# Performance work log

Measured on AMD Instinct MI355X. Metric: run time of the kernel, lower is better.

Reference implementation:

```python
import jax, jax.numpy as jnp
import numpy as np

jax.config.update("jax_enable_x64", True)  # hash uses int64 (prime * coord ~ 7e12)

FEATURE_DIM = 2
GRID_DIM = 3
NUM_LVL = 16
MAX_RES = 2048
MIN_RES = 16
HASH_POWER = 19
MAX_ENTRY = 2 ** HASH_POWER
PRIMES = (3367900313, 2654435761, 805459861)

_b = np.exp((np.log(MAX_RES) - np.log(MIN_RES)) / (NUM_LVL - 1))
RESOLUTIONS = [int(np.floor(MIN_RES * _b ** i)) for i in range(NUM_LVL)]
TABLE_SIZES = [min(r ** GRID_DIM, MAX_ENTRY) for r in RESOLUTIONS]

# Corner offset order matches get_corner(): [c000, c010, c001, c011, c100, c101, c110, c111]
OFFSETS = np.array([[0, 0, 0], [0, 1, 0], [0, 0, 1], [0, 1, 1],
                    [1, 0, 0], [1, 0, 1], [1, 1, 0], [1, 1, 1]], dtype=np.int64)

N = 1 << 20  # number of query points


def setup_inputs() -> dict:
    key = jax.random.key(0)
    kx, kt = jax.random.split(key)
    x = jax.random.uniform(kx, (N, GRID_DIM), dtype=jnp.float32)  # in [0,1]
    # stacked (padded) hashtables; dense levels only use their first res^3 rows
    tables = jax.random.normal(kt, (NUM_LVL, MAX_ENTRY, FEATURE_DIM), dtype=jnp.float32) * 1e-4
    return {"x": x, "tables": tables}


def _level(x, table, res, table_size):
    resf = float(res)
    coord = jnp.clip(x * (resf - 1.0), 0.0, resf - 1.0001)  # [N,3] hash-space coords
    fl = jnp.floor(coord)
    corners = fl.astype(jnp.int64)[:, None, :] + jnp.asarray(OFFSETS)  # [N,8,3]
    if table_size != MAX_ENTRY:
        # dense spatial index: sum_i c_i * res^i
        idx = corners[..., 0] + corners[..., 1] * res + corners[..., 2] * (res * res)
    else:
        # NGP hash: xor of coord*prime, mod table size
        h = (corners[..., 0] * PRIMES[0]) ^ (corners[..., 1] * PRIMES[1]) ^ (corners[..., 2] * PRIMES[2])
        idx = h % MAX_ENTRY
    feat = table[idx]  # [N,8,F] gather
    d = coord - fl  # fractional part, [N,3]
    xx, yy, zz = d[:, 0], d[:, 1], d[:, 2]
    mx, my, mz = 1.0 - xx, 1.0 - yy, 1.0 - zz
    # weight order matches interpolation_weights() stack order
    w = jnp.stack([mx * my * mz, xx * my * mz, mx * yy * mz, xx * yy * mz,
                   mx * my * zz, xx * my * zz, mx * yy * zz, xx * yy * zz], axis=-1)  # [N,8]
    return (feat * w[..., None]).sum(axis=-2)  # [N,F]


def reference(x, tables):
    outs = [_level(x, tables[l], RESOLUTIONS[l], TABLE_SIZES[l]) for l in range(NUM_LVL)]
    return jnp.concatenate(outs, axis=-1)  # [N, NUM_LVL*FEATURE_DIM]
```

## Files before the change

kernel.cpp:

```cpp
#include <hip/hip_runtime.h>
#include <math.h>

#define NLVL 16
#define MAX_ENTRY (1 << 19)
#define NPTS (1 << 20)

typedef float f2_t __attribute__((ext_vector_type(2)));
typedef float f4_t __attribute__((ext_vector_type(4)));

__device__ __forceinline__ void nt_store2(float2 v, float2* p) {
    f2_t t; t.x = v.x; t.y = v.y;
    __builtin_nontemporal_store(t, (f2_t*)p);
}
__device__ __forceinline__ void nt_store4(float4 v, float4* p) {
    f4_t t; t.x = v.x; t.y = v.y; t.z = v.z; t.w = v.w;
    __builtin_nontemporal_store(t, (f4_t*)p);
}
__device__ __forceinline__ void nt_storeu(unsigned v, unsigned* p) {
    __builtin_nontemporal_store(v, p);
}
__device__ __forceinline__ float4 nt_load4(const float4* p) {
    f4_t t = __builtin_nontemporal_load((const f4_t*)p);
    return make_float4(t.x, t.y, t.z, t.w);
}
__device__ __forceinline__ unsigned nt_loadu(const unsigned* p) {
    return __builtin_nontemporal_load(p);
}

__device__ __forceinline__ unsigned pack_bf16(float a, float b) {
    unsigned ua = __float_as_uint(a), ub = __float_as_uint(b);
    ua = (ua + 0x7FFFu + ((ua >> 16) & 1u)) >> 16;
    ub = (ub + 0x7FFFu + ((ub >> 16) & 1u)) >> 16;
    return ua | (ub << 16);
}
__device__ __forceinline__ float bf_lo(unsigned u) { return __uint_as_float(u << 16); }
__device__ __forceinline__ float bf_hi(unsigned u) { return __uint_as_float(u & 0xFFFF0000u); }

__device__ __constant__ int OX[8] = {0, 0, 0, 0, 1, 1, 1, 1};
__device__ __constant__ int OY[8] = {0, 1, 0, 1, 0, 0, 1, 1};
__device__ __constant__ int OZ[8] = {0, 0, 1, 1, 0, 1, 0, 1};

__device__ __forceinline__ void corner_setup(
    float x0, float x1, float x2, float s, float hi,
    int& cx, int& cy, int& cz,
    float (&wx)[2], float (&wy)[2], float (&wz)[2])
{
    float c0 = fminf(fmaxf(x0 * s, 0.0f), hi);
    float c1 = fminf(fmaxf(x1 * s, 0.0f), hi);
    float c2 = fminf(fmaxf(x2 * s, 0.0f), hi);
    float f0 = floorf(c0), f1 = floorf(c1), f2 = floorf(c2);
    cx = (int)f0; cy = (int)f1; cz = (int)f2;
    float xx = c0 - f0, yy = c1 - f1, zz = c2 - f2;
    wx[0] = 1.0f - xx; wx[1] = xx;
    wy[0] = 1.0f - yy; wy[1] = yy;
    wz[0] = 1.0f - zz; wz[1] = zz;
}

__device__ __forceinline__ void acc_pair(
    int j, float4 f, const float (&wx)[2], const float (&wy)[2], const float (&wz)[2],
    float& a0, float& a1)
{
    const float w0 = wx[j & 1] * wy[j >> 1] * wz[0];
    const float w1 = wx[j >> 1] * wy[j & 1] * wz[1];
    a0 += w0 * f.x + w1 * f.z;
    a1 += w0 * f.y + w1 * f.w;
}

struct OptP {
    int   res[NLVL];
    int   res2[NLVL];
    float scale[NLVL];
    float hi[NLVL];
    int   cdim1, cdim2, cdim3;
};


__global__ __launch_bounds__(256) void repack2_kernel(
    const float* __restrict__ x,
    const float* __restrict__ tables,
    float4* __restrict__ blk1,
    float4* __restrict__ blk2,
    float4* __restrict__ blk3,
    float4* __restrict__ xp,
    OptP P)
{
    const long long stride = (long long)gridDim.x * 256;
    const long long tid = (long long)blockIdx.x * 256 + threadIdx.x;

#pragma unroll
    for (int l = 1; l <= 2; ++l) {
        const int res = P.res[l], res2v = P.res2[l];
        const int cdim = res - 1;
        const long long ncell = (long long)cdim * cdim * cdim;
        const float2* tab = (const float2*)(tables + (size_t)l * MAX_ENTRY * 2);
        float4* dst = (l == 1) ? blk1 : blk2;
        for (long long c = tid; c < ncell; c += stride) {
            const int cx = (int)(c % cdim);
            const int cy = (int)((c / cdim) % cdim);
            const int cz = (int)(c / ((long long)cdim * cdim));
            const int base = cx + cy * res + cz * res2v;
#pragma unroll
            for (int j = 0; j < 4; ++j) {
                const int oy = j & 1, oz = j >> 1;
                const float2 e0 = tab[base + oy * res + oz * res2v];
                const float2 e1 = tab[base + 1 + oy * res + oz * res2v];
                nt_store4(make_float4(e0.x, e0.y, e1.x, e1.y), &dst[c * 4 + j]);
            }
        }
    }

    {
        const int res = P.res[3], res2v = P.res2[3];
        const int cdim = P.cdim3;
        const long long nblk = (long long)cdim * cdim * res;
        const float2* tab = (const float2*)(tables + (size_t)3 * MAX_ENTRY * 2);
        for (long long b = tid; b < nblk; b += stride) {
            const int bx = (int)(b % cdim);
            const int by = (int)((b / cdim) % cdim);
            const int z  = (int)(b / ((long long)cdim * cdim));
            const int base = bx + by * res + z * res2v;
#pragma unroll
            for (int oy = 0; oy < 2; ++oy) {
                const float2 e0 = tab[base + oy * res];
                const float2 e1 = tab[base + 1 + oy * res];
                nt_store4(make_float4(e0.x, e0.y, e1.x, e1.y), &blk3[b * 2 + oy]);
            }
        }
    }

    for (long long i = tid; i < NPTS; i += stride) {
        xp[i] = make_float4(x[3 * i + 0], x[3 * i + 1], x[3 * i + 2], 0.0f);
    }
}

__global__ __launch_bounds__(256) void passA_kernel(
    const float4* __restrict__ xp,
    const float* __restrict__ tables,
    const float4* __restrict__ blk1,
    const float4* __restrict__ blk2,
    unsigned* __restrict__ fb,
    OptP P)
{
    __shared__ float2 lds0[4096];
    {
        const float2* tab0 = (const float2*)tables;
        for (int j = threadIdx.x; j < 4096; j += 256) lds0[j] = tab0[j];
    }
    __syncthreads();

    const int i = blockIdx.x * 256 + threadIdx.x;

    const float4 v = nt_load4(&xp[i]);
    const float x0 = v.x, x1 = v.y, x2 = v.z;

    {
        int cx, cy, cz;
        float wx[2], wy[2], wz[2];
        corner_setup(x0, x1, x2, P.scale[0], P.hi[0], cx, cy, cz, wx, wy, wz);
        const int res = P.res[0], res2v = P.res2[0];
        const int base = cx + cy * res + cz * res2v;
        float a0 = 0.0f, a1 = 0.0f;
#pragma unroll
        for (int k = 0; k < 8; ++k) {
            const int idx = base + OX[k] + OY[k] * res + OZ[k] * res2v;
            const float2 f = lds0[idx];
            const float w = wx[k & 1] * wy[(k >> 1) & 1] * wz[k >> 2];
            a0 += w * f.x; a1 += w * f.y;
        }
        nt_storeu(pack_bf16(a0, a1), &fb[i]);
    }

#pragma unroll
    for (int l = 1; l <= 2; ++l) {
        int cx, cy, cz;
        float wx[2], wy[2], wz[2];
        corner_setup(x0, x1, x2, P.scale[l], P.hi[l], cx, cy, cz, wx, wy, wz);
        const int cdim = (l == 1) ? P.cdim1 : P.cdim2;
        const float4* blk = (l == 1) ? blk1 : blk2;
        const long long c = cx + (long long)cy * cdim + (long long)cz * cdim * cdim;
        float a0 = 0.0f, a1 = 0.0f;
#pragma unroll
        for (int j = 0; j < 4; ++j) {
            const float4 f = blk[c * 4 + j];
            acc_pair(j, f, wx, wy, wz, a0, a1);
        }
        nt_storeu(pack_bf16(a0, a1), &fb[(size_t)l * NPTS + i]);
    }
}

__global__ __launch_bounds__(256) void mega_kernel(
    const float4* __restrict__ xp,
    const float* __restrict__ tables,
    const float4* __restrict__ blk3,
    unsigned* __restrict__ fb,
    OptP P)
{
    const int seg = blockIdx.x >> 11;
    const int lvl = seg + 3;
    const int t = (blockIdx.x & 2047) * 256 + threadIdx.x;
    unsigned* fbl = fb + (size_t)lvl * NPTS;

    const float scale = P.scale[lvl], hiv = P.hi[lvl];

#pragma unroll
    for (int h = 0; h < 2; ++h) {
        const int i = t + h * (NPTS / 2);
        const float4 v = nt_load4(&xp[i]);
        int cx, cy, cz;
        float wx[2], wy[2], wz[2];
        corner_setup(v.x, v.y, v.z, scale, hiv, cx, cy, cz, wx, wy, wz);

        float a0 = 0.0f, a1 = 0.0f;

        if (lvl == 3) {
            const int cdim = P.cdim3;
            const long long b0 = cx + (long long)cy * cdim + (long long)cz * cdim * cdim;
            const long long b1 = b0 + (long long)cdim * cdim;
#pragma unroll
            for (int oz = 0; oz < 2; ++oz) {
                const long long b = (oz == 0) ? b0 : b1;
#pragma unroll
                for (int oy = 0; oy < 2; ++oy) {
                    const float4 f = blk3[b * 2 + oy];
                    acc_pair(oy + 2 * oz, f, wx, wy, wz, a0, a1);
                }
            }
        } else if (lvl < 6) {
            const int res = P.res[lvl], res2v = P.res2[lvl];
            const float2* tab = (const float2*)tables + (size_t)lvl * MAX_ENTRY;
            const int base = cx + cy * res + cz * res2v;
#pragma unroll
            for (int j = 0; j < 4; ++j) {
                const int idx = base + (j & 1) * res + (j >> 1) * res2v;
                const float2 flo = tab[idx];
                const float2 fhi = tab[idx + 1];
                acc_pair(j, make_float4(flo.x, flo.y, fhi.x, fhi.y), wx, wy, wz, a0, a1);
            }
        } else {
            const float2* tab = (const float2*)tables + (size_t)lvl * MAX_ENTRY;
            const unsigned P0 = 3367900313u, P1 = 2654435761u, P2 = 805459861u;
            unsigned hx[2], hy[2], hz[2];
            hx[0] = (unsigned)cx * P0; hx[1] = hx[0] + P0;
            hy[0] = (unsigned)cy * P1; hy[1] = hy[0] + P1;
            hz[0] = (unsigned)cz * P2; hz[1] = hz[0] + P2;
#pragma unroll
            for (int k = 0; k < 8; ++k) {
                const unsigned idx = (hx[OX[k]] ^ hy[OY[k]] ^ hz[OZ[k]]) & (MAX_ENTRY - 1);
                const float2 f = tab[idx];
                const float w = wx[k & 1] * wy[(k >> 1) & 1] * wz[k >> 2];
                a0 += w * f.x; a1 += w * f.y;
            }
        }

        nt_storeu(pack_bf16(a0, a1), &fbl[i]);
    }
}

__global__ __launch_bounds__(256) void assemble_bf_kernel(
    const unsigned* __restrict__ fb, float4* __restrict__ out)
{
    const size_t tid = (size_t)blockIdx.x * 256 + threadIdx.x;
    const int    c   = (int)(tid & 7);
    const size_t p   = tid >> 3;
    const unsigned u0 = nt_loadu(&fb[(size_t)(2 * c) * NPTS + p]);
    const unsigned u1 = nt_loadu(&fb[(size_t)(2 * c + 1) * NPTS + p]);
    nt_store4(make_float4(bf_lo(u0), bf_hi(u0), bf_lo(u1), bf_hi(u1)), &out[tid]);
}


struct DenseParams {
    int   res[6];
    int   res2[6];
    float scale[6];
    float hi[6];
    long long tab_off[6];
};

__device__ __forceinline__ float2 hash_point_fb(
    float x0, float x1, float x2, const float2* __restrict__ tab,
    float scale, float hi)
{
    int cx, cy, cz;
    float wx[2], wy[2], wz[2];
    corner_setup(x0, x1, x2, scale, hi, cx, cy, cz, wx, wy, wz);
    const unsigned P0 = 3367900313u, P1 = 2654435761u, P2 = 805459861u;
    unsigned hx[2], hy[2], hz[2];
    hx[0] = (unsigned)cx * P0; hx[1] = hx[0] + P0;
    hy[0] = (unsigned)cy * P1; hy[1] = hy[0] + P1;
    hz[0] = (unsigned)cz * P2; hz[1] = hz[0] + P2;
    float a0 = 0.0f, a1 = 0.0f;
#pragma unroll
    for (int k = 0; k < 8; ++k) {
        const unsigned idx = (hx[OX[k]] ^ hy[OY[k]] ^ hz[OZ[k]]) & (MAX_ENTRY - 1);
        const float2 f = tab[idx];
        const float w = wx[k & 1] * wy[(k >> 1) & 1] * wz[k >> 2];
        a0 += w * f.x; a1 += w * f.y;
    }
    return make_float2(a0, a1);
}

__global__ __launch_bounds__(256) void dense6_kernel(
    const float* __restrict__ x,
    const float* __restrict__ tables,
    float* __restrict__ out,
    DenseParams P)
{
    const int i = blockIdx.x * 256 + threadIdx.x;
    if (i >= NPTS) return;
    const float x0 = x[3 * i + 0];
    const float x1 = x[3 * i + 1];
    const float x2 = x[3 * i + 2];
    float o[12];
#pragma unroll
    for (int l = 0; l < 6; ++l) {
        int cx, cy, cz;
        float wx[2], wy[2], wz[2];
        corner_setup(x0, x1, x2, P.scale[l], P.hi[l], cx, cy, cz, wx, wy, wz);
        const float2* tab = (const float2*)(tables + P.tab_off[l]);
        const int res  = P.res[l];
        const int res2 = P.res2[l];
        const int base = cx + cy * res + cz * res2;
        float a0 = 0.0f, a1 = 0.0f;
#pragma unroll
        for (int k = 0; k < 8; ++k) {
            const int idx = base + OX[k] + OY[k] * res + OZ[k] * res2;
            const float2 f = tab[idx];
            const float w = wx[k & 1] * wy[(k >> 1) & 1] * wz[k >> 2];
            a0 += w * f.x; a1 += w * f.y;
        }
        o[2 * l + 0] = a0; o[2 * l + 1] = a1;
    }
    float4* op = (float4*)(out + (size_t)i * 32);
    op[0] = ((float4*)o)[0];
    op[1] = ((float4*)o)[1];
    op[2] = ((float4*)o)[2];
}

__global__ __launch_bounds__(256) void hash_level_kernel(
    const float* __restrict__ x,
    const float* __restrict__ tables,
    float* __restrict__ out,
    int level, float scale, float hi)
{
    const int i = blockIdx.x * 256 + threadIdx.x;
    if (i >= NPTS) return;
    const float2* tab = (const float2*)tables + (size_t)level * MAX_ENTRY;
    const float2 r = hash_point_fb(x[3 * i], x[3 * i + 1], x[3 * i + 2], tab, scale, hi);
    *(float2*)(out + (size_t)i * 32 + 2 * level) = r;
}

__global__ __launch_bounds__(256) void generic_level_kernel(
    const float* __restrict__ x,
    const float* __restrict__ tables,
    float* __restrict__ out,
    int level, int res, int res2, int use_hash, float scale, float hi)
{
    const int i = blockIdx.x * 256 + threadIdx.x;
    if (i >= NPTS) return;
    const float x0 = x[3 * i + 0];
    const float x1 = x[3 * i + 1];
    const float x2 = x[3 * i + 2];
    int cx, cy, cz;
    float wx[2], wy[2], wz[2];
    corner_setup(x0, x1, x2, scale, hi, cx, cy, cz, wx, wy, wz);
    const float2* tab = (const float2*)tables + (size_t)level * MAX_ENTRY;
    float a0 = 0.0f, a1 = 0.0f;
    if (use_hash) {
        const unsigned P0 = 3367900313u, P1 = 2654435761u, P2 = 805459861u;
        unsigned hx[2], hy[2], hz[2];
        hx[0] = (unsigned)cx * P0; hx[1] = hx[0] + P0;
        hy[0] = (unsigned)cy * P1; hy[1] = hy[0] + P1;
        hz[0] = (unsigned)cz * P2; hz[1] = hz[0] + P2;
#pragma unroll
        for (int k = 0; k < 8; ++k) {
            const unsigned idx = (hx[OX[k]] ^ hy[OY[k]] ^ hz[OZ[k]]) & (MAX_ENTRY - 1);
            const float2 f = tab[idx];
            const float w = wx[k & 1] * wy[(k >> 1) & 1] * wz[k >> 2];
            a0 += w * f.x; a1 += w * f.y;
        }
    } else {
        const int base = cx + cy * res + cz * res2;
#pragma unroll
        for (int k = 0; k < 8; ++k) {
            const int idx = base + OX[k] + OY[k] * res + OZ[k] * res2;
            const float2 f = tab[idx];
            const float w = wx[k & 1] * wy[(k >> 1) & 1] * wz[k >> 2];
            a0 += w * f.x; a1 += w * f.y;
        }
    }
    *(float2*)(out + (size_t)i * 32 + 2 * level) = make_float2(a0, a1);
}


extern "C" void kernel_launch(void* const* d_in, const int* in_sizes, int n_in,
                              void* d_out, int out_size, void* d_ws, size_t ws_size,
                              hipStream_t stream)
{
    const float* x      = (const float*)d_in[0];
    const float* tables = (const float*)d_in[1];
    float* out          = (float*)d_out;

    int   res[NLVL], res2[NLVL], use_hash[NLVL];
    float scale[NLVL], hi[NLVL];
    const double b = exp((log(2048.0) - log(16.0)) / 15.0);
    for (int l = 0; l < NLVL; ++l) {
        const int r = (int)floor(16.0 * pow(b, (double)l));
        res[l]  = r;
        res2[l] = r * r;
        const long long t3 = (long long)r * r * r;
        use_hash[l] = (t3 >= (long long)MAX_ENTRY) ? 1 : 0;
        scale[l] = (float)(r - 1);
        hi[l]    = (float)((double)r - 1.0001);
    }

    const int block = 256;
    const int grid  = (NPTS + block - 1) / block;

    bool expected = true;
    for (int l = 0; l < 6; ++l)    expected = expected && !use_hash[l];
    for (int l = 6; l < NLVL; ++l) expected = expected && use_hash[l];
    expected = expected && (res[0] * res[0] * res[0] <= 4096);

    const int cdim1 = res[1] - 1, cdim2 = res[2] - 1, cdim3 = res[3] - 1;
    const size_t sz1 = (size_t)cdim1 * cdim1 * cdim1 * 64;
    const size_t sz2 = (size_t)cdim2 * cdim2 * cdim2 * 64;
    const size_t sz3 = (size_t)cdim3 * cdim3 * res[3] * 32;
    auto al = [](size_t v) { return (v + 255) & ~(size_t)255; };
    const size_t off1 = 0;
    const size_t off2 = al(off1 + sz1);
    const size_t off3 = al(off2 + sz2);
    const size_t offxp = al(off3 + sz3);
    const size_t offfb = al(offxp + (size_t)NPTS * 16);
    const size_t need = offfb + (size_t)NLVL * NPTS * 4;

    if (expected && ws_size >= need) {
        float4* blk1 = (float4*)((char*)d_ws + off1);
        float4* blk2 = (float4*)((char*)d_ws + off2);
        float4* blk3 = (float4*)((char*)d_ws + off3);
        float4* xp   = (float4*)((char*)d_ws + offxp);
        unsigned* fb = (unsigned*)((char*)d_ws + offfb);

        OptP P;
        for (int l = 0; l < NLVL; ++l) {
            P.res[l] = res[l]; P.res2[l] = res2[l];
            P.scale[l] = scale[l]; P.hi[l] = hi[l];
        }
        P.cdim1 = cdim1; P.cdim2 = cdim2; P.cdim3 = cdim3;

        repack2_kernel<<<1024, block, 0, stream>>>(x, tables, blk1, blk2, blk3, xp, P);
        passA_kernel<<<grid, block, 0, stream>>>(xp, tables, blk1, blk2, fb, P);
        mega_kernel<<<13 * 2048, block, 0, stream>>>(xp, tables, blk3, fb, P);
        assemble_bf_kernel<<<(NPTS * 8) / block, block, 0, stream>>>(fb, (float4*)out);
    } else if (expected) {
        DenseParams P;
        for (int l = 0; l < 6; ++l) {
            P.res[l] = res[l]; P.res2[l] = res2[l];
            P.scale[l] = scale[l]; P.hi[l] = hi[l];
            P.tab_off[l] = (long long)l * MAX_ENTRY * 2;
        }
        dense6_kernel<<<grid, block, 0, stream>>>(x, tables, out, P);
        for (int l = 6; l < NLVL; ++l) {
            hash_level_kernel<<<grid, block, 0, stream>>>(x, tables, out, l, scale[l], hi[l]);
        }
    } else {
        for (int l = 0; l < NLVL; ++l) {
            generic_level_kernel<<<grid, block, 0, stream>>>(
                x, tables, out, l, res[l], res2[l], use_hash[l], scale[l], hi[l]);
        }
    }
}
```

Measured before the change: 602.1 us.

## Use nontemporal table loads, LDS-transpose assemble, and double repack grid

Switches the table and block gathers in passA and the mega kernel to nontemporal loads. Rewrites the final assemble kernel to stage 512 points of all 16 bf16 levels in LDS, then write the interleaved float4 output, so each global read is contiguous. Doubles the repack grid size. Nontemporal hints on randomly gathered tables may reduce cache reuse, since hashed and dense lookups hit repeated entries.

```diff
diff --git a/kernel.cpp b/kernel.cpp
--- a/kernel.cpp
+++ b/kernel.cpp
@@ -8,16 +8,16 @@
 typedef float f2_t __attribute__((ext_vector_type(2)));
 typedef float f4_t __attribute__((ext_vector_type(4)));
 
-__device__ __forceinline__ void nt_store2(float2 v, float2* p) {
-    f2_t t; t.x = v.x; t.y = v.y;
-    __builtin_nontemporal_store(t, (f2_t*)p);
-}
 __device__ __forceinline__ void nt_store4(float4 v, float4* p) {
     f4_t t; t.x = v.x; t.y = v.y; t.z = v.z; t.w = v.w;
     __builtin_nontemporal_store(t, (f4_t*)p);
 }
 __device__ __forceinline__ void nt_storeu(unsigned v, unsigned* p) {
     __builtin_nontemporal_store(v, p);
+}
+__device__ __forceinline__ float2 nt_load2(const float2* p) {
+    f2_t t = __builtin_nontemporal_load((const f2_t*)p);
+    return make_float2(t.x, t.y);
 }
 __device__ __forceinline__ float4 nt_load4(const float4* p) {
     f4_t t = __builtin_nontemporal_load((const f4_t*)p);
@@ -181,7 +181,7 @@
         float a0 = 0.0f, a1 = 0.0f;
 #pragma unroll
         for (int j = 0; j < 4; ++j) {
-            const float4 f = blk[c * 4 + j];
+            const float4 f = nt_load4(&blk[c * 4 + j]);
             acc_pair(j, f, wx, wy, wz, a0, a1);
         }
         nt_storeu(pack_bf16(a0, a1), &fb[(size_t)l * NPTS + i]);
@@ -221,7 +221,7 @@
                 const long long b = (oz == 0) ? b0 : b1;
 #pragma unroll
                 for (int oy = 0; oy < 2; ++oy) {
-                    const float4 f = blk3[b * 2 + oy];
+                    const float4 f = nt_load4(&blk3[b * 2 + oy]);
                     acc_pair(oy + 2 * oz, f, wx, wy, wz, a0, a1);
                 }
             }
@@ -232,8 +232,8 @@
 #pragma unroll
             for (int j = 0; j < 4; ++j) {
                 const int idx = base + (j & 1) * res + (j >> 1) * res2v;
-                const float2 flo = tab[idx];
-                const float2 fhi = tab[idx + 1];
+                const float2 flo = nt_load2(&tab[idx]);
+                const float2 fhi = nt_load2(&tab[idx + 1]);
                 acc_pair(j, make_float4(flo.x, flo.y, fhi.x, fhi.y), wx, wy, wz, a0, a1);
             }
         } else {
@@ -246,7 +246,7 @@
 #pragma unroll
             for (int k = 0; k < 8; ++k) {
                 const unsigned idx = (hx[OX[k]] ^ hy[OY[k]] ^ hz[OZ[k]]) & (MAX_ENTRY - 1);
-                const float2 f = tab[idx];
+                const float2 f = nt_load2(&tab[idx]);
                 const float w = wx[k & 1] * wy[(k >> 1) & 1] * wz[k >> 2];
                 a0 += w * f.x; a1 += w * f.y;
             }
@@ -256,15 +256,32 @@
     }
 }
 
-__global__ __launch_bounds__(256) void assemble_bf_kernel(
+#define ASM_PTS 512
+#define ASM_STRIDE 514
+__global__ __launch_bounds__(256) void assemble_t_kernel(
     const unsigned* __restrict__ fb, float4* __restrict__ out)
 {
-    const size_t tid = (size_t)blockIdx.x * 256 + threadIdx.x;
-    const int    c   = (int)(tid & 7);
-    const size_t p   = tid >> 3;
-    const unsigned u0 = nt_loadu(&fb[(size_t)(2 * c) * NPTS + p]);
-    const unsigned u1 = nt_loadu(&fb[(size_t)(2 * c + 1) * NPTS + p]);
-    nt_store4(make_float4(bf_lo(u0), bf_hi(u0), bf_lo(u1), bf_hi(u1)), &out[tid]);
+    __shared__ unsigned lds[NLVL * ASM_STRIDE];
+    const int base = blockIdx.x * ASM_PTS;
+    const int tid = threadIdx.x;
+
+#pragma unroll
+    for (int l = 0; l < NLVL; ++l) {
+        lds[l * ASM_STRIDE + tid]       = nt_loadu(&fb[(size_t)l * NPTS + base + tid]);
+        lds[l * ASM_STRIDE + 256 + tid] = nt_loadu(&fb[(size_t)l * NPTS + base + 256 + tid]);
+    }
+    __syncthreads();
+
+    float4* o4 = out + (size_t)base * 8;
+#pragma unroll
+    for (int j = 0; j < 16; ++j) {
+        const int g = j * 256 + tid;
+        const int p = g >> 3;
+        const int c = g & 7;
+        const unsigned u0 = lds[(2 * c) * ASM_STRIDE + p];
+        const unsigned u1 = lds[(2 * c + 1) * ASM_STRIDE + p];
+        nt_store4(make_float4(bf_lo(u0), bf_hi(u0), bf_lo(u1), bf_hi(u1)), &o4[g]);
+    }
 }
 
 
@@ -447,10 +464,10 @@
         }
         P.cdim1 = cdim1; P.cdim2 = cdim2; P.cdim3 = cdim3;
 
-        repack2_kernel<<<1024, block, 0, stream>>>(x, tables, blk1, blk2, blk3, xp, P);
+        repack2_kernel<<<2048, block, 0, stream>>>(x, tables, blk1, blk2, blk3, xp, P);
         passA_kernel<<<grid, block, 0, stream>>>(xp, tables, blk1, blk2, fb, P);
         mega_kernel<<<13 * 2048, block, 0, stream>>>(xp, tables, blk3, fb, P);
-        assemble_bf_kernel<<<(NPTS * 8) / block, block, 0, stream>>>(fb, (float4*)out);
+        assemble_t_kernel<<<NPTS / ASM_PTS, block, 0, stream>>>(fb, (float4*)out);
     } else if (expected) {
         DenseParams P;
         for (int l = 0; l < 6; ++l) {
```

New measurement: 1.319 ms. 119% more time.
